# Optimization experiments

Measured on AMD Instinct MI355X. Metric: run time of the kernel, lower is better.

## Reference

```python
import jax, jax.numpy as jnp
import numpy as np

N_BALLS = 256
BATCH = 128
N_STEPS = 100
MAX_EVENTS = 5
WORLD_W = 10.0
WORLD_H = 10.0
RADIUS = 0.1
HID = 64
DT = 0.05
INF = jnp.float32(1e30)

_II_np, _JJ_np = np.triu_indices(N_BALLS, 1)
_II = jnp.asarray(_II_np)
_JJ = jnp.asarray(_JJ_np)
# wall order: left, right, bottom, top (normals point into the box)
_WN = jnp.array([[1.0, 0.0], [-1.0, 0.0], [0.0, 1.0], [0.0, -1.0]], dtype=jnp.float32)
_WP = jnp.array([0.0, -WORLD_W, 0.0, -WORLD_H], dtype=jnp.float32)


def setup_inputs():
    key = jax.random.key(0)
    ks = jax.random.split(key, 6)
    pos = jax.random.uniform(ks[0], (BATCH, N_BALLS, 2), minval=0.5, maxval=9.5)
    vel = jax.random.normal(ks[1], (BATCH, N_BALLS, 2))
    state = jnp.concatenate([pos, vel], axis=-1)  # [B, N, 4]
    radii = jnp.full((N_BALLS,), RADIUS, dtype=jnp.float32)
    sc = 0.1
    W1 = jax.random.normal(ks[2], (HID, 2)) * sc
    b1 = jnp.zeros((HID,), jnp.float32)
    W2 = jax.random.normal(ks[3], (HID, HID)) * sc
    b2 = jnp.zeros((HID,), jnp.float32)
    W3 = jax.random.normal(ks[4], (1, HID)) * sc
    b3 = jnp.zeros((1,), jnp.float32)
    return {"state": state, "radii": radii, "W1": W1, "b1": b1, "W2": W2,
            "b2": b2, "W3": W3, "b3": b3, "dt": DT, "n_steps": N_STEPS}


def _detect(pos, vel, radii):
    # pos, vel: [N,2]; vectorized replacement of the Python O(N^2) loop.
    diff = pos[_JJ] - pos[_II]                       # [P,2]
    dist = jnp.linalg.norm(diff, axis=-1)            # [P]
    gap_b = dist - (radii[_II] + radii[_JJ])
    nhat = diff / (dist + 1e-8)[:, None]
    app_b = jnp.sum((vel[_JJ] - vel[_II]) * nhat, axis=-1)
    gb = jnp.where(app_b < 0, gap_b, INF)            # only approaching pairs
    r = radii
    gw = jnp.stack([pos[:, 0] - r, WORLD_W - pos[:, 0] - r,
                    pos[:, 1] - r, WORLD_H - pos[:, 1] - r], axis=-1)  # [N,4]
    vw = jnp.stack([vel[:, 0] < 0, vel[:, 0] > 0,
                    vel[:, 1] < 0, vel[:, 1] > 0], axis=-1)
    gw = jnp.where(vw, gw, INF)
    allg = jnp.concatenate([gb, gw.reshape(-1)])
    k = jnp.argmin(allg)
    P = gb.shape[0]
    is_ball = k < P
    gap = allg[k]
    bi = jnp.where(is_ball, k, 0)
    i_b, j_b = _II[bi], _JJ[bi]
    kw = jnp.where(is_ball, 0, k - P)
    i_w, wid = kw // 4, kw % 4
    return gap, is_ball, i_b, j_b, i_w, wid


def _apply_jump(s, i, j, W1, b1, W2, b2, W3, b3):
    pos, vel = s[..., :2], s[..., 2:]
    diff = pos[:, j] - pos[:, i]                               # [B,2]
    dist = jnp.maximum(jnp.linalg.norm(diff, axis=-1, keepdims=True), 1e-8)
    nhat = diff / dist
    app = jnp.sum((vel[:, j] - vel[:, i]) * nhat, axis=-1, keepdims=True)
    h = jnp.concatenate([dist, app], axis=-1)                  # [B,2]
    h = jax.nn.silu(h @ W1.T + b1)
    h = jax.nn.silu(h @ W2.T + b2)
    imp = (h @ W3.T + b3) * nhat                               # [B,2]
    vel_new = vel.at[:, i].add(imp).at[:, j].add(-imp)
    return jnp.concatenate([pos, vel_new], axis=-1)


def _apply_wall(s, i, wn, wp, r):
    pos, vel = s[..., :2], s[..., 2:]
    v, p = vel[:, i], pos[:, i]
    vn = jnp.sum(v * wn, axis=-1, keepdims=True)
    vel_new = vel.at[:, i].set(v - 2.0 * vn * wn)
    pn = jnp.sum(p * wn, axis=-1, keepdims=True)
    pen = jnp.maximum(wp + r - pn, 0.0)
    pos_new = pos.at[:, i].set(p + pen * wn)
    return jnp.concatenate([pos_new, vel_new], axis=-1)


def _rollout(state, radii, W1, b1, W2, b2, W3, b3, dt, n_steps):
    dt = jnp.float32(dt)

    def event_body(_, carry):
        curr, t_c, t_e, done = carry
        pos0, vel0 = curr[0, :, :2], curr[0, :, 2:]
        gap, is_ball, i_b, j_b, i_w, wid = _detect(pos0, vel0, radii)
        no_event = gap > 0.05
        n = pos0[j_b] - pos0[i_b]
        app_ball = -jnp.sum((vel0[j_b] - vel0[i_b]) * n / jnp.linalg.norm(n))
        app_wall = jnp.abs(jnp.max(vel0[i_w]))
        app = jnp.where(is_ball, app_ball, app_wall)
        t_ev = t_c + gap / jnp.maximum(app, 1e-6)
        # ZeroFlow is constant velocity -> dopri5 integrate is exact linear drift
        dte = jnp.where(t_ev > t_c + 1e-10, t_ev - t_c, 0.0)

        def apply_map(s):
            jm = _apply_jump(s, i_b, j_b, W1, b1, W2, b2, W3, b3)
            wm = _apply_wall(s, i_w, _WN[wid], _WP[wid], radii[i_w])
            return jnp.where(is_ball, jm, wm)

        state_a = apply_map(curr)                       # gap <= 0: jump now
        integ = curr.at[..., :2].add(curr[..., 2:] * dte)
        state_b = apply_map(integ)                      # 0 < gap: drift then jump
        act = (~done) & (~no_event)
        case_a = act & (gap <= 0)
        case_b = act & (gap > 0) & (app > 1e-6) & (t_ev < t_e)
        new_done = done | no_event | (act & (gap > 0) & ((app <= 1e-6) | (t_ev >= t_e)))
        new_curr = jnp.where(case_a, state_a, jnp.where(case_b, state_b, curr))
        new_t_c = jnp.where(case_b, t_ev, t_c)
        return new_curr, new_t_c, t_e, new_done

    def step(curr, step_idx):
        t_s = step_idx.astype(jnp.float32) * dt
        t_e = t_s + dt
        curr, t_c, _, _ = jax.lax.fori_loop(
            0, MAX_EVENTS, event_body, (curr, t_s, t_e, jnp.bool_(False)))
        dte = jnp.where(t_e > t_c + 1e-10, t_e - t_c, 0.0)
        curr = curr.at[..., :2].add(curr[..., 2:] * dte)
        return curr, curr

    _, traj = jax.lax.scan(step, state, jnp.arange(n_steps))
    return jnp.concatenate([state[None], traj], axis=0)   # [n_steps+1, B, N, 4]


def reference(state, radii, W1, b1, W2, b2, W3, b3, dt, n_steps):
    return _rollout(state, radii, W1, b1, W2, b2, W3, b3, dt, n_steps)
```

## Files before the change

kernel.cpp:

```cpp
#include <hip/hip_runtime.h>
#include <stdint.h>

#define NB 256
#define NBATCH 128
#define HID 64
#define MAXEV 5
#define MAXSTEPS 256
#define NT 43
#define NTILES 946
#define W2S 65
#define CAND_MAX 6144
#define CMARGIN 1.5f
#define NTHR 512
#define D2GATE 0.0626f

typedef unsigned long long u64;

__device__ __forceinline__ float bf2f(unsigned short u) {
    return __uint_as_float(((unsigned)u) << 16);
}
__device__ __forceinline__ unsigned short f2bf(float f) {
    unsigned u = __float_as_uint(f);
    u += 0x7FFFu + ((u >> 16) & 1u);
    return (unsigned short)(u >> 16);
}
__device__ __forceinline__ float rdin(const void* p, int idx, int bf) {
    return bf ? bf2f(((const unsigned short*)p)[idx]) : ((const float*)p)[idx];
}
__device__ __forceinline__ float silu_f(float x) {
    float s = __fdiv_rn(1.0f, __fadd_rn(1.0f, expf(-x)));
    return __fmul_rn(x, s);
}
__device__ __forceinline__ void lds_fence() {
    __builtin_amdgcn_wave_barrier();
    __threadfence_block();
    __builtin_amdgcn_wave_barrier();
}
__device__ __forceinline__ unsigned fmap(float g) {
    unsigned u = __float_as_uint(g);
    unsigned m = (unsigned)(((int)u) >> 31) | 0x80000000u;
    return u ^ m;
}
__device__ __forceinline__ float funmap(unsigned sb) {
    unsigned u = (sb & 0x80000000u) ? (sb ^ 0x80000000u) : ~sb;
    return __uint_as_float(u);
}

template<int CTRL>
__device__ __forceinline__ u64 dpp_min_u64_step(u64 k) {
    unsigned lo = (unsigned)k, hi = (unsigned)(k >> 32);
    unsigned nlo = (unsigned)__builtin_amdgcn_update_dpp(-1, (int)lo, CTRL, 0xF, 0xF, false);
    unsigned nhi = (unsigned)__builtin_amdgcn_update_dpp(-1, (int)hi, CTRL, 0xF, 0xF, false);
    u64 nk = (((u64)nhi) << 32) | (u64)nlo;
    return nk < k ? nk : k;
}
__device__ __forceinline__ u64 wave_min_u64(u64 k) {
    k = dpp_min_u64_step<0x111>(k);
    k = dpp_min_u64_step<0x112>(k);
    k = dpp_min_u64_step<0x114>(k);
    k = dpp_min_u64_step<0x118>(k);
    k = dpp_min_u64_step<0x142>(k);
    k = dpp_min_u64_step<0x143>(k);
    unsigned lo = (unsigned)__builtin_amdgcn_readlane((int)(unsigned)k, 63);
    unsigned hi = (unsigned)__builtin_amdgcn_readlane((int)(unsigned)(k >> 32), 63);
    return (((u64)hi) << 32) | (u64)lo;
}
template<int CTRL>
__device__ __forceinline__ float dpp_max_f32_step(float x) {
    int nx = __builtin_amdgcn_update_dpp(0, __float_as_int(x), CTRL, 0xF, 0xF, false);
    return fmaxf(x, __int_as_float(nx));
}
__device__ __forceinline__ float wave_max_f32(float x) {
    x = dpp_max_f32_step<0x111>(x);
    x = dpp_max_f32_step<0x112>(x);
    x = dpp_max_f32_step<0x114>(x);
    x = dpp_max_f32_step<0x118>(x);
    x = dpp_max_f32_step<0x142>(x);
    x = dpp_max_f32_step<0x143>(x);
    return __int_as_float(__builtin_amdgcn_readlane(__float_as_int(x), 63));
}

__device__ __forceinline__ void append_agg(unsigned* list, int* counter, int cap, unsigned val) {
    u64 m = __ballot(1);
    int lane = (int)(threadIdx.x & 63);
    int ldr = (int)__builtin_ctzll(m);
    int pfx = (int)__builtin_popcountll(m & ((1ull << lane) - 1ull));
    int base = 0;
    if (lane == ldr) base = atomicAdd(counter, (int)__builtin_popcountll(m));
    base = __builtin_amdgcn_readfirstlane(base);
    int idx = base + pfx;
    if (idx < cap) list[idx] = val;
}

__device__ __forceinline__ u64 ball_key(const float4* ps, int i, int j,
                                        float dx, float dy, float d2,
                                        unsigned id, float rsum) {
    float4 A = ps[i], B = ps[j];
    float p1 = __fmul_rn(__fsub_rn(B.z, A.z), dx);
    float p2 = __fmul_rn(__fsub_rn(B.w, A.w), dy);
    float dot = __fadd_rn(p1, p2);
    float mag = __fadd_rn(fabsf(p1), fabsf(p2));
    bool appr;
    if (fabsf(dot) < __fmul_rn(1e-5f, mag)) {
        float dist = __fsqrt_rn(d2);
        float den = __fadd_rn(dist, 1e-8f);
        float ab = __fadd_rn(__fmul_rn(__fsub_rn(B.z, A.z), __fdiv_rn(dx, den)),
                             __fmul_rn(__fsub_rn(B.w, A.w), __fdiv_rn(dy, den)));
        appr = ab < 0.0f;
    } else {
        appr = dot < 0.0f;
    }
    if (!appr) return ~0ull;
    float gap = __fsub_rn(__fsqrt_rn(d2), rsum);
    return (((u64)fmap(gap)) << 17) | id;
}

__device__ __forceinline__ void scan_list(const unsigned* src, int n,
                                          const float2* pos2c, const float4* ps0c,
                                          float rsum, u64& kC, int tid) {
    unsigned idq[8];
    #pragma unroll
    for (int q = 0; q < 8; q++) {
        int c = tid + q * NTHR;
        idq[q] = (c < n) ? src[c] : 0u;
    }
    float2 Aq[8], Bq[8];
    #pragma unroll
    for (int q = 0; q < 8; q++) {
        Aq[q] = pos2c[idq[q] >> 8];
        Bq[q] = pos2c[idq[q] & 255u];
    }
    #pragma unroll
    for (int q = 0; q < 8; q++) {
        float dx = __fsub_rn(Bq[q].x, Aq[q].x), dy = __fsub_rn(Bq[q].y, Aq[q].y);
        float d2 = __fadd_rn(__fmul_rn(dx, dx), __fmul_rn(dy, dy));
        bool live = (tid + q * NTHR) < n;
        if (live && d2 < D2GATE) {
            u64 key = ball_key(ps0c, (int)(idq[q] >> 8), (int)(idq[q] & 255u),
                               dx, dy, d2, idq[q], rsum);
            kC = key < kC ? key : kC;
        }
    }
    for (int c = tid + 8 * NTHR; c < n; c += NTHR) {
        unsigned id = src[c];
        float2 A = pos2c[id >> 8], B = pos2c[id & 255u];
        float dx = __fsub_rn(B.x, A.x), dy = __fsub_rn(B.y, A.y);
        float d2 = __fadd_rn(__fmul_rn(dx, dx), __fmul_rn(dy, dy));
        if (d2 < D2GATE) {
            u64 key = ball_key(ps0c, (int)(id >> 8), (int)(id & 255u), dx, dy, d2, id, rsum);
            kC = key < kC ? key : kC;
        }
    }
}

__device__ __forceinline__ void scan_full(const float2* pos2c, const float4* ps0c, float rsum,
                                          int i0a, int j0a, int i0b, int j0b,
                                          bool apB, float th2B, unsigned* cand, int* candN,
                                          u64& kC) {
    #pragma unroll
    for (int tt = 0; tt < 2; tt++) {
        int I0 = tt ? i0b : i0a;
        int J0 = tt ? j0b : j0a;
        if (I0 < 0) continue;
        float2 Pi[6], Pj[6];
        #pragma unroll
        for (int a = 0; a < 6; a++) {
            int ii = I0 + a; ii = ii < NB ? ii : NB - 1;
            int jj = J0 + a; jj = jj < NB ? jj : NB - 1;
            Pi[a] = pos2c[ii]; Pj[a] = pos2c[jj];
        }
        #pragma unroll
        for (int a = 0; a < 6; a++) {
            int i = I0 + a;
            #pragma unroll
            for (int bb = 0; bb < 6; bb++) {
                int j = J0 + bb;
                bool ok = (i < NB) && (j < NB) && (j > i);
                float dx = __fsub_rn(Pj[bb].x, Pi[a].x);
                float dy = __fsub_rn(Pj[bb].y, Pi[a].y);
                float d2 = __fadd_rn(__fmul_rn(dx, dx), __fmul_rn(dy, dy));
                unsigned id = (unsigned)((i << 8) | j);
                if (apB && ok && d2 < th2B) append_agg(cand, candN, CAND_MAX, id);
                if (ok && d2 < D2GATE) {
                    u64 key = ball_key(ps0c, i, j, dx, dy, d2, id, rsum);
                    kC = key < kC ? key : kC;
                }
            }
        }
    }
}

__device__ __forceinline__ void store_ball(void* out, long long base, int t, float4 Q, int bf) {
    if (bf) {
        ushort4 v;
        v.x = f2bf(Q.x); v.y = f2bf(Q.y); v.z = f2bf(Q.z); v.w = f2bf(Q.w);
        ((ushort4*)((unsigned short*)out + base))[t] = v;
    } else {
        ((float4*)((float*)out + base))[t] = Q;
    }
}

__device__ void load_weights(float* w1, float* b1s, float* w2, float* b2s, float* w3, float* b3s,
                             const void* W1, const void* B1, const void* W2, const void* B2,
                             const void* W3, const void* B3, int bf, int tid, int nthr) {
    for (int k = tid; k < HID * 2; k += nthr) w1[k] = rdin(W1, k, bf);
    for (int k = tid; k < HID; k += nthr) {
        b1s[k] = rdin(B1, k, bf);
        b2s[k] = rdin(B2, k, bf);
        w3[k]  = rdin(W3, k, bf);
    }
    for (int k = tid; k < HID * HID; k += nthr) {
        int m = k >> 6, c = k & 63;
        w2[m * W2S + c] = rdin(W2, k, bf);
    }
    if (tid == 0) b3s[0] = rdin(B3, 0, bf);
}

__global__ void sniff_kernel(const unsigned short* st, int* ws) {
    __shared__ int ev;
    if (threadIdx.x == 0) ev = 0;
    __syncthreads();
    unsigned short u = st[threadIdx.x];
    int e = (u >> 7) & 0xFF;
    if (e >= 0x85) atomicOr(&ev, 1);
    __syncthreads();
    if (threadIdx.x == 0) ws[0] = ev ? 0 : 1;
}

__global__ void row0_kernel(const void* in, void* out, const int* ws) {
    int idx = blockIdx.x * blockDim.x + threadIdx.x;
    if (ws[0]) ((unsigned short*)out)[idx] = ((const unsigned short*)in)[idx];
    else       ((float*)out)[idx] = ((const float*)in)[idx];
}

__global__ __launch_bounds__(NTHR, 1) void sim_kernel(
    const void* in_state, const void* in_rad,
    const void* inW1, const void* inB1, const void* inW2, const void* inB2,
    const void* inW3, const void* inB3, const void* in_dt, const int* in_nsteps,
    void* out, const int* ws) {
    __shared__ float4 ps0[2][NB];
    __shared__ float4 psb[2][NB];
    __shared__ float2 pos2[2][NB];
    __shared__ float w1[HID * 2], b1s[HID], w2[HID * W2S], b2s[HID], w3s[HID], b3s[1];
    __shared__ float sc0[132], scb[132];
    __shared__ u64 redK[8];
    __shared__ float redF[5];
    __shared__ unsigned cand[CAND_MAX];
    __shared__ int candN;
    __shared__ int pubF;
    __shared__ int rebF;

    int tid = threadIdx.x;
    int b = blockIdx.x;
    int bf = ws[0];

    if (tid < NB) {
        int base0 = tid * 4;
        float4 P;
        P.x = rdin(in_state, base0 + 0, bf);
        P.y = rdin(in_state, base0 + 1, bf);
        P.z = rdin(in_state, base0 + 2, bf);
        P.w = rdin(in_state, base0 + 3, bf);
        ps0[0][tid] = P;
        float2 p2v; p2v.x = P.x; p2v.y = P.y;
        pos2[0][tid] = p2v;
        int baseb = (b * NB + tid) * 4;
        float4 Q;
        Q.x = rdin(in_state, baseb + 0, bf);
        Q.y = rdin(in_state, baseb + 1, bf);
        Q.z = rdin(in_state, baseb + 2, bf);
        Q.w = rdin(in_state, baseb + 3, bf);
        psb[0][tid] = Q;
        float m2 = P.z * P.z + P.w * P.w;
        m2 = wave_max_f32(m2);
        if ((tid & 63) == 0) redF[tid >> 6] = m2;
    }
    load_weights(w1, b1s, w2, b2s, w3s, b3s, inW1, inB1, inW2, inB2, inW3, inB3, bf, tid, NTHR);
    if (tid == 0) { candN = 0; pubF = 0; rebF = 1; redF[4] = 0.0f; }

    float dtv = rdin(in_dt, 0, bf);
    int NS = in_nsteps[0]; if (NS > MAXSTEPS) NS = MAXSTEPS; if (NS < 0) NS = 0;
    float rad0 = rdin(in_rad, 0, bf);
    float rsum = __fadd_rn(rad0, rad0);

    int i0a = -1, j0a = 0, i0b = -1, j0b = 0;
    {
        int T = tid;
        if (T < NTILES) {
            int rem = T, r = 0;
            while (rem >= NT - r) { rem -= NT - r; r++; }
            i0a = r * 6; j0a = (r + rem) * 6;
        }
        T = tid + NTHR;
        if (T < NTILES) {
            int rem = T, r = 0;
            while (rem >= NT - r) { rem -= NT - r; r++; }
            i0b = r * 6; j0b = (r + rem) * 6;
        }
    }
    __syncthreads();

    float thB = __fadd_rn(__fadd_rn(rsum, 0.05f), CMARGIN);
    float th2B = __fmul_rn(thB, thB);

    int p = 0;
    int nc = 0;
    bool candOvf = false;
    float used = 1e30f, vcap = 0.0f;

    for (int s = 0; s < NS; s++) {
        int rebuild = rebF;
        float t_s = __fmul_rn((float)s, dtv);
        float t_e = __fadd_rn(t_s, dtv);
        float t_c = t_s;
        long long obase = ((long long)(s + 1) * NBATCH + b) * (NB * 4);
        if (tid < 64) {
            if (rebuild) {
                vcap = sqrtf(fmaxf(fmaxf(fmaxf(redF[0], redF[1]),
                                         fmaxf(redF[2], redF[3])), redF[4]));
                used = 0.0f;
            }
            used = __fadd_rn(used, __fmul_rn(__fmul_rn(2.0f, dtv), vcap));
        }

        for (int e = 0; e < MAXEV; e++) {
            const float4* ps0c = ps0[p];
            const float2* pos2c = pos2[p];
            const float4* psbc = psb[p];
            float4* ps0n = ps0[p ^ 1];
            float2* pos2n = pos2[p ^ 1];
            float4* psbn = psb[p ^ 1];

            u64 kC = ~0ull;
            int mode;
            if (e == 0) mode = rebuild ? 2 : 1;
            else        mode = pubF ? 2 : 1;
            if (mode == 2) {
                bool apB = (e == 0);
                scan_full(pos2c, ps0c, rsum, i0a, j0a, i0b, j0b,
                          apB, th2B, cand, &candN, kC);
            } else {
                scan_list(cand, nc, pos2c, ps0c, rsum, kC, tid);
            }
            {
                int ball = tid & 255, wsel = tid >> 8;
                float4 P = ps0c[ball];
                #pragma unroll
                for (int q = 0; q < 2; q++) {
                    int w = wsel * 2 + q;
                    float g; bool valid;
                    if (w == 0)      { g = __fsub_rn(P.x, rad0); valid = P.z < 0.0f; }
                    else if (w == 1) { g = __fsub_rn(__fsub_rn(10.0f, P.x), rad0); valid = P.z > 0.0f; }
                    else if (w == 2) { g = __fsub_rn(P.y, rad0); valid = P.w < 0.0f; }
                    else             { g = __fsub_rn(__fsub_rn(10.0f, P.y), rad0); valid = P.w > 0.0f; }
                    if (valid) {
                        u64 key = (((u64)fmap(g)) << 17) | 0x10000u | (unsigned)(ball * 4 + w);
                        kC = key < kC ? key : kC;
                    }
                }
            }
            kC = wave_min_u64(kC);
            if ((tid & 63) == 0) redK[tid >> 6] = kC;
            __syncthreads();

            if (e == 0 && rebuild) {
                int ct = candN;
                candOvf = ct > CAND_MAX;
                nc = candOvf ? CAND_MAX : ct;
            }

            float g_nx = 0, g_ny = 0, g_dist = 0, g_app = 0;
            float4 gA, gB;
            int code = 0; float dteB = 0.0f; float tcn = t_c;
            int ei = 0, ejw = 0;
            {
                u64 m = redK[0];
                #pragma unroll
                for (int q = 1; q < 8; q++) m = redK[q] < m ? redK[q] : m;
                if (m != ~0ull) {
                    bool is_ball = ((m >> 16) & 1ull) == 0;
                    unsigned id = (unsigned)(m & 0xFFFFull);
                    float gap = funmap((unsigned)(m >> 17));
                    int pi = (int)(id >> 8), pj = (int)(id & 255u);
                    int wb = (int)(id >> 2), ww = (int)(id & 3u);
                    ei = is_ball ? pi : wb;
                    ejw = is_ball ? pj : ww;
                    float4 A, B;
                    if (!(gap > 0.05f)) {
                        float app;
                        if (is_ball) {
                            A = ps0c[pi]; B = ps0c[pj];
                            float dx = __fsub_rn(B.x, A.x), dy = __fsub_rn(B.y, A.y);
                            float nrm = __fsqrt_rn(__fadd_rn(__fmul_rn(dx, dx), __fmul_rn(dy, dy)));
                            float dvx = __fsub_rn(B.z, A.z), dvy = __fsub_rn(B.w, A.w);
                            app = -__fadd_rn(__fdiv_rn(__fmul_rn(dvx, dx), nrm),
                                             __fdiv_rn(__fmul_rn(dvy, dy), nrm));
                        } else {
                            float4 Wb = ps0c[wb];
                            app = fabsf(fmaxf(Wb.z, Wb.w));
                        }
                        float t_ev = __fadd_rn(t_c, __fdiv_rn(gap, fmaxf(app, 1e-6f)));
                        if (gap <= 0.0f) {
                            code = is_ball ? 1 : 3;
                        } else if (app > 1e-6f && t_ev < t_e) {
                            code = is_ball ? 2 : 4;
                            dteB = (t_ev > __fadd_rn(t_c, 1e-10f)) ? __fsub_rn(t_ev, t_c) : 0.0f;
                            tcn = t_ev;
                        }
                    }
                    if (tid < 64 && code != 0 && code <= 2) {
                        if (code == 2) {
                            A.x = __fadd_rn(A.x, __fmul_rn(A.z, dteB));
                            A.y = __fadd_rn(A.y, __fmul_rn(A.w, dteB));
                            B.x = __fadd_rn(B.x, __fmul_rn(B.z, dteB));
                            B.y = __fadd_rn(B.y, __fmul_rn(B.w, dteB));
                        }
                        gA = A; gB = B;
                        float dx = __fsub_rn(B.x, A.x), dy = __fsub_rn(B.y, A.y);
                        float nrm = __fsqrt_rn(__fadd_rn(__fmul_rn(dx, dx), __fmul_rn(dy, dy)));
                        float dist = fmaxf(nrm, 1e-8f);
                        g_nx = __fdiv_rn(dx, dist); g_ny = __fdiv_rn(dy, dist);
                        g_dist = dist;
                        float dvx = __fsub_rn(B.z, A.z), dvy = __fsub_rn(B.w, A.w);
                        g_app = __fadd_rn(__fmul_rn(dvx, g_nx), __fmul_rn(dvy, g_ny));
                    }
                }
            }

            if (code == 0) {
                float fd = (t_e > __fadd_rn(t_c, 1e-10f)) ? __fsub_rn(t_e, t_c) : 0.0f;
                if (tid < NB) {
                    float4 P = ps0c[tid];
                    P.x = __fadd_rn(P.x, __fmul_rn(P.z, fd));
                    P.y = __fadd_rn(P.y, __fmul_rn(P.w, fd));
                    ps0n[tid] = P;
                    float2 pp; pp.x = P.x; pp.y = P.y; pos2n[tid] = pp;
                    float m2 = P.z * P.z + P.w * P.w;
                    m2 = wave_max_f32(m2);
                    if ((tid & 63) == 0) redF[tid >> 6] = m2;
                    if (tid == 0) {
                        redF[4] = 0.0f;
                        candN = 0;
                        float usedNext = __fadd_rn(used, __fmul_rn(__fmul_rn(2.0f, dtv), vcap));
                        rebF = (candOvf || (__fadd_rn(usedNext, 1e-3f) > CMARGIN)) ? 1 : 0;
                    }
                } else {
                    int t = tid - NB;
                    float4 Q = psbc[t];
                    Q.x = __fadd_rn(Q.x, __fmul_rn(Q.z, fd));
                    Q.y = __fadd_rn(Q.y, __fmul_rn(Q.w, fd));
                    psbn[t] = Q;
                    store_ball(out, obase, t, Q, bf);
                }
                __syncthreads();
                p ^= 1;
                break;
            }

            t_c = tcn;
            bool integ = (code == 2) || (code == 4);
            bool last = (e == MAXEV - 1);
            float fd = 0.0f;
            if (last) fd = (t_e > __fadd_rn(t_c, 1e-10f)) ? __fsub_rn(t_e, t_c) : 0.0f;
            int skip2 = (code <= 2) ? ejw : -1;

            if (code <= 2) {
                if (tid < 64) {
                    float a = __fadd_rn(__fadd_rn(__fmul_rn(g_dist, w1[2 * tid]),
                                                  __fmul_rn(g_app, w1[2 * tid + 1])), b1s[tid]);
                    sc0[4 + tid] = silu_f(a);
                    lds_fence();
                    float acc = 0.0f;
                    const float* row = &w2[tid * W2S];
                    #pragma unroll 8
                    for (int k = 0; k < HID; k++) acc = __fadd_rn(acc, __fmul_rn(sc0[4 + k], row[k]));
                    acc = __fadd_rn(acc, b2s[tid]);
                    sc0[68 + tid] = silu_f(acc);
                    lds_fence();
                    float acc3 = 0.0f;
                    #pragma unroll 8
                    for (int k = 0; k < HID; k++)
                        acc3 = __fadd_rn(acc3, __fmul_rn(sc0[68 + k], w3s[k]));
                    float impv = __fadd_rn(acc3, b3s[0]);
                    float ix = __fmul_rn(impv, g_nx), iy = __fmul_rn(impv, g_ny);
                    float nAz = __fadd_rn(gA.z, ix),  nAw = __fadd_rn(gA.w, iy);
                    float nBz = __fadd_rn(gB.z, -ix), nBw = __fadd_rn(gB.w, -iy);
                    if (tid == 0) {
                        float4 outA; outA.x = gA.x; outA.y = gA.y; outA.z = nAz; outA.w = nAw;
                        float4 outB; outB.x = gB.x; outB.y = gB.y; outB.z = nBz; outB.w = nBw;
                        if (last) {
                            outA.x = __fadd_rn(outA.x, __fmul_rn(outA.z, fd));
                            outA.y = __fadd_rn(outA.y, __fmul_rn(outA.w, fd));
                            outB.x = __fadd_rn(outB.x, __fmul_rn(outB.z, fd));
                            outB.y = __fadd_rn(outB.y, __fmul_rn(outB.w, fd));
                        }
                        ps0n[ei] = outA; ps0n[ejw] = outB;
                        float2 pa; pa.x = outA.x; pa.y = outA.y; pos2n[ei] = pa;
                        float2 pb; pb.x = outB.x; pb.y = outB.y; pos2n[ejw] = pb;
                    }
                    float s1 = sqrtf(nAz * nAz + nAw * nAw);
                    float s2 = sqrtf(nBz * nBz + nBw * nBw);
                    float nv = fmaxf(s1, s2);
                    used = __fadd_rn(used, __fmul_rn(__fmul_rn(2.0f, dtv),
                                                     fmaxf(__fsub_rn(nv, vcap), 0.0f)));
                    vcap = fmaxf(vcap, nv);
                    int nf = (candOvf || (__fadd_rn(used, 1e-3f) > CMARGIN)) ? 1 : 0;
                    if (tid == 0) {
                        pubF = nf;
                        if (last) {
                            redF[4] = fmaxf(nAz * nAz + nAw * nAw, nBz * nBz + nBw * nBw);
                            candN = 0;
                            float usedNext = __fadd_rn(used, __fmul_rn(__fmul_rn(2.0f, dtv), vcap));
                            rebF = (candOvf || (__fadd_rn(usedNext, 1e-3f) > CMARGIN)) ? 1 : 0;
                        }
                    }
                } else if (tid < 128) {
                    int lane = tid - 64;
                    float4 A = psbc[ei], B = psbc[ejw];
                    if (integ) {
                        A.x = __fadd_rn(A.x, __fmul_rn(A.z, dteB));
                        A.y = __fadd_rn(A.y, __fmul_rn(A.w, dteB));
                        B.x = __fadd_rn(B.x, __fmul_rn(B.z, dteB));
                        B.y = __fadd_rn(B.y, __fmul_rn(B.w, dteB));
                    }
                    float dx = __fsub_rn(B.x, A.x), dy = __fsub_rn(B.y, A.y);
                    float nrm = __fsqrt_rn(__fadd_rn(__fmul_rn(dx, dx), __fmul_rn(dy, dy)));
                    float dist = fmaxf(nrm, 1e-8f);
                    float nx = __fdiv_rn(dx, dist), ny = __fdiv_rn(dy, dist);
                    float dvx = __fsub_rn(B.z, A.z), dvy = __fsub_rn(B.w, A.w);
                    float app2 = __fadd_rn(__fmul_rn(dvx, nx), __fmul_rn(dvy, ny));
                    float a = __fadd_rn(__fadd_rn(__fmul_rn(dist, w1[2 * lane]),
                                                  __fmul_rn(app2, w1[2 * lane + 1])), b1s[lane]);
                    scb[4 + lane] = silu_f(a);
                    lds_fence();
                    float acc = 0.0f;
                    const float* row = &w2[lane * W2S];
                    #pragma unroll 8
                    for (int k = 0; k < HID; k++) acc = __fadd_rn(acc, __fmul_rn(scb[4 + k], row[k]));
                    acc = __fadd_rn(acc, b2s[lane]);
                    scb[68 + lane] = silu_f(acc);
                    lds_fence();
                    float acc3 = 0.0f;
                    #pragma unroll 8
                    for (int k = 0; k < HID; k++)
                        acc3 = __fadd_rn(acc3, __fmul_rn(scb[68 + k], w3s[k]));
                    float impv = __fadd_rn(acc3, b3s[0]);
                    if (lane == 0) {
                        float ix = __fmul_rn(impv, nx), iy = __fmul_rn(impv, ny);
                        float4 outA; outA.x = A.x; outA.y = A.y;
                        outA.z = __fadd_rn(A.z, ix);  outA.w = __fadd_rn(A.w, iy);
                        float4 outB; outB.x = B.x; outB.y = B.y;
                        outB.z = __fadd_rn(B.z, -ix); outB.w = __fadd_rn(B.w, -iy);
                        if (last) {
                            outA.x = __fadd_rn(outA.x, __fmul_rn(outA.z, fd));
                            outA.y = __fadd_rn(outA.y, __fmul_rn(outA.w, fd));
                            outB.x = __fadd_rn(outB.x, __fmul_rn(outB.z, fd));
                            outB.y = __fadd_rn(outB.y, __fmul_rn(outB.w, fd));
                            store_ball(out, obase, ei, outA, bf);
                            store_ball(out, obase, ejw, outB, bf);
                        }
                        psbn[ei] = outA; psbn[ejw] = outB;
                    }
                }
            } else {
                const float wnx[4] = {1.f, -1.f, 0.f, 0.f};
                const float wny[4] = {0.f, 0.f, 1.f, -1.f};
                const float wpv[4] = {0.f, -10.f, 0.f, -10.f};
                int w = ejw;
                if (tid < 64) {
                    float4 P = ps0c[ei];
                    if (integ) {
                        P.x = __fadd_rn(P.x, __fmul_rn(P.z, dteB));
                        P.y = __fadd_rn(P.y, __fmul_rn(P.w, dteB));
                    }
                    float vn = __fadd_rn(__fmul_rn(P.z, wnx[w]), __fmul_rn(P.w, wny[w]));
                    float t2 = __fmul_rn(2.0f, vn);
                    float nvx = __fsub_rn(P.z, __fmul_rn(t2, wnx[w]));
                    float nvy = __fsub_rn(P.w, __fmul_rn(t2, wny[w]));
                    float pn = __fadd_rn(__fmul_rn(P.x, wnx[w]), __fmul_rn(P.y, wny[w]));
                    float pen = fmaxf(__fsub_rn(__fadd_rn(wpv[w], rad0), pn), 0.0f);
                    float4 nP;
                    nP.x = __fadd_rn(P.x, __fmul_rn(pen, wnx[w]));
                    nP.y = __fadd_rn(P.y, __fmul_rn(pen, wny[w]));
                    nP.z = nvx; nP.w = nvy;
                    if (last) {
                        nP.x = __fadd_rn(nP.x, __fmul_rn(nP.z, fd));
                        nP.y = __fadd_rn(nP.y, __fmul_rn(nP.w, fd));
                    }
                    used = __fadd_rn(used, pen);
                    int nf = (candOvf || (__fadd_rn(used, 1e-3f) > CMARGIN)) ? 1 : 0;
                    if (tid == 0) {
                        ps0n[ei] = nP;
                        float2 pp; pp.x = nP.x; pp.y = nP.y; pos2n[ei] = pp;
                        pubF = nf;
                        if (last) {
                            redF[4] = nvx * nvx + nvy * nvy;
                            candN = 0;
                            float usedNext = __fadd_rn(used, __fmul_rn(__fmul_rn(2.0f, dtv), vcap));
                            rebF = (candOvf || (__fadd_rn(usedNext, 1e-3f) > CMARGIN)) ? 1 : 0;
                        }
                    }
                } else if (tid < 128) {
                    if (tid == 64) {
                        float4 P = psbc[ei];
                        if (integ) {
                            P.x = __fadd_rn(P.x, __fmul_rn(P.z, dteB));
                            P.y = __fadd_rn(P.y, __fmul_rn(P.w, dteB));
                        }
                        float vn = __fadd_rn(__fmul_rn(P.z, wnx[w]), __fmul_rn(P.w, wny[w]));
                        float t2 = __fmul_rn(2.0f, vn);
                        float nvx = __fsub_rn(P.z, __fmul_rn(t2, wnx[w]));
                        float nvy = __fsub_rn(P.w, __fmul_rn(t2, wny[w]));
                        float pn = __fadd_rn(__fmul_rn(P.x, wnx[w]), __fmul_rn(P.y, wny[w]));
                        float pen = fmaxf(__fsub_rn(__fadd_rn(wpv[w], rad0), pn), 0.0f);
                        float4 nP;
                        nP.x = __fadd_rn(P.x, __fmul_rn(pen, wnx[w]));
                        nP.y = __fadd_rn(P.y, __fmul_rn(pen, wny[w]));
                        nP.z = nvx; nP.w = nvy;
                        if (last) {
                            nP.x = __fadd_rn(nP.x, __fmul_rn(nP.z, fd));
                            nP.y = __fadd_rn(nP.y, __fmul_rn(nP.w, fd));
                            store_ball(out, obase, ei, nP, bf);
                        }
                        psbn[ei] = nP;
                    }
                }
            }
            if (tid >= 128 && tid < 384) {
                int t = tid - 128;
                float m2 = 0.0f;
                if (t != ei && t != skip2) {
                    float4 P = ps0c[t];
                    P.x = __fadd_rn(P.x, __fmul_rn(P.z, dteB));
                    P.y = __fadd_rn(P.y, __fmul_rn(P.w, dteB));
                    if (last) {
                        P.x = __fadd_rn(P.x, __fmul_rn(P.z, fd));
                        P.y = __fadd_rn(P.y, __fmul_rn(P.w, fd));
                        m2 = P.z * P.z + P.w * P.w;
                    }
                    ps0n[t] = P;
                    float2 pp; pp.x = P.x; pp.y = P.y; pos2n[t] = pp;
                }
                if (last) {
                    float mx = wave_max_f32(m2);
                    if ((tid & 63) == 0) redF[(tid >> 6) - 2] = mx;
                }
            } else if (tid >= 384) {
                #pragma unroll
                for (int q = 0; q < 2; q++) {
                    int t = (tid - 384) + q * 128;
                    if (t != ei && t != skip2) {
                        float4 Q = psbc[t];
                        Q.x = __fadd_rn(Q.x, __fmul_rn(Q.z, dteB));
                        Q.y = __fadd_rn(Q.y, __fmul_rn(Q.w, dteB));
                        if (last) {
                            Q.x = __fadd_rn(Q.x, __fmul_rn(Q.z, fd));
                            Q.y = __fadd_rn(Q.y, __fmul_rn(Q.w, fd));
                            store_ball(out, obase, t, Q, bf);
                        }
                        psbn[t] = Q;
                    }
                }
            }
            __syncthreads();
            p ^= 1;
        }
    }
}

extern "C" void kernel_launch(void* const* d_in, const int* in_sizes, int n_in,
                              void* d_out, int out_size, void* d_ws, size_t ws_size,
                              hipStream_t stream) {
    int* ws = (int*)d_ws;
    sniff_kernel<<<1, 256, 0, stream>>>((const unsigned short*)d_in[0], ws);
    row0_kernel<<<(NBATCH * NB * 4) / 256, 256, 0, stream>>>(d_in[0], d_out, ws);
    sim_kernel<<<NBATCH, NTHR, 0, stream>>>(
        d_in[0], d_in[1], d_in[2], d_in[3], d_in[4], d_in[5], d_in[6], d_in[7],
        d_in[8], (const int*)d_in[9], d_out, ws);
}
```

Baseline: 3.261 ms.

## Prescan next event's candidate pairs during state update to drop a barrier

Candidate-list and wall keys for the next event are now computed speculatively during the current update phase, using predicted positions, and written into a double-buffered reduction array. The next event then reads that precomputed minimum and only rescans pairs and walls involving the one or two balls that just changed. The separate float2 position array is removed and ball_key reads are taken from register float4s. This aims to remove one full scan and one __syncthreads per event, in exchange for more work and register pressure in the update phase and some risk of mismatch between predicted and actual positions.

```diff
diff --git a/kernel.cpp b/kernel.cpp
--- a/kernel.cpp
+++ b/kernel.cpp
@@ -92,10 +92,8 @@
     if (idx < cap) list[idx] = val;
 }
 
-__device__ __forceinline__ u64 ball_key(const float4* ps, int i, int j,
-                                        float dx, float dy, float d2,
-                                        unsigned id, float rsum) {
-    float4 A = ps[i], B = ps[j];
+__device__ __forceinline__ u64 ball_key_v(float4 A, float4 B, float dx, float dy,
+                                          float d2, unsigned id, float rsum) {
     float p1 = __fmul_rn(__fsub_rn(B.z, A.z), dx);
     float p2 = __fmul_rn(__fsub_rn(B.w, A.w), dy);
     float dot = __fadd_rn(p1, p2);
@@ -115,59 +113,91 @@
     return (((u64)fmap(gap)) << 17) | id;
 }
 
-__device__ __forceinline__ void scan_list(const unsigned* src, int n,
-                                          const float2* pos2c, const float4* ps0c,
-                                          float rsum, u64& kC, int tid) {
-    unsigned idq[8];
+__device__ __forceinline__ u64 wall_keys2(float px, float py, float vz, float vw,
+                                          float rad0, int ball, int wsel) {
+    u64 k = ~0ull;
     #pragma unroll
-    for (int q = 0; q < 8; q++) {
-        int c = tid + q * NTHR;
-        idq[q] = (c < n) ? src[c] : 0u;
-    }
-    float2 Aq[8], Bq[8];
-    #pragma unroll
-    for (int q = 0; q < 8; q++) {
-        Aq[q] = pos2c[idq[q] >> 8];
-        Bq[q] = pos2c[idq[q] & 255u];
-    }
-    #pragma unroll
-    for (int q = 0; q < 8; q++) {
-        float dx = __fsub_rn(Bq[q].x, Aq[q].x), dy = __fsub_rn(Bq[q].y, Aq[q].y);
-        float d2 = __fadd_rn(__fmul_rn(dx, dx), __fmul_rn(dy, dy));
-        bool live = (tid + q * NTHR) < n;
-        if (live && d2 < D2GATE) {
-            u64 key = ball_key(ps0c, (int)(idq[q] >> 8), (int)(idq[q] & 255u),
-                               dx, dy, d2, idq[q], rsum);
-            kC = key < kC ? key : kC;
-        }
-    }
-    for (int c = tid + 8 * NTHR; c < n; c += NTHR) {
-        unsigned id = src[c];
-        float2 A = pos2c[id >> 8], B = pos2c[id & 255u];
-        float dx = __fsub_rn(B.x, A.x), dy = __fsub_rn(B.y, A.y);
-        float d2 = __fadd_rn(__fmul_rn(dx, dx), __fmul_rn(dy, dy));
-        if (d2 < D2GATE) {
-            u64 key = ball_key(ps0c, (int)(id >> 8), (int)(id & 255u), dx, dy, d2, id, rsum);
-            kC = key < kC ? key : kC;
-        }
-    }
-}
-
-__device__ __forceinline__ void scan_full(const float2* pos2c, const float4* ps0c, float rsum,
-                                          int i0a, int j0a, int i0b, int j0b,
-                                          bool apB, float th2B, unsigned* cand, int* candN,
-                                          u64& kC) {
+    for (int q = 0; q < 2; q++) {
+        int w = wsel * 2 + q;
+        float g; bool valid;
+        if (w == 0)      { g = __fsub_rn(px, rad0); valid = vz < 0.0f; }
+        else if (w == 1) { g = __fsub_rn(__fsub_rn(10.0f, px), rad0); valid = vz > 0.0f; }
+        else if (w == 2) { g = __fsub_rn(py, rad0); valid = vw < 0.0f; }
+        else             { g = __fsub_rn(__fsub_rn(10.0f, py), rad0); valid = vw > 0.0f; }
+        if (valid) {
+            u64 key = (((u64)fmap(g)) << 17) | 0x10000u | (unsigned)(ball * 4 + w);
+            k = key < k ? key : k;
+        }
+    }
+    return k;
+}
+__device__ __forceinline__ u64 wall_keys4(float4 P, float rad0, int ball) {
+    u64 k = wall_keys2(P.x, P.y, P.z, P.w, rad0, ball, 0);
+    u64 k2 = wall_keys2(P.x, P.y, P.z, P.w, rad0, ball, 1);
+    return k2 < k ? k2 : k;
+}
+
+__device__ __forceinline__ void pred_pos(float4 P, float dta, float dtb, bool dtbon,
+                                         float& px, float& py) {
+    px = __fadd_rn(P.x, __fmul_rn(P.z, dta));
+    py = __fadd_rn(P.y, __fmul_rn(P.w, dta));
+    if (dtbon) {
+        px = __fadd_rn(px, __fmul_rn(P.z, dtb));
+        py = __fadd_rn(py, __fmul_rn(P.w, dtb));
+    }
+}
+
+__device__ __forceinline__ void prescan_pairs(const unsigned* cand, int n,
+        const float4* ps0c, int e0, int e1, float dta, float dtb, bool dtbon,
+        float rsum, u64& kC, int start, int stride) {
+    for (int c0 = start; c0 < n; c0 += stride * 4) {
+        unsigned id4[4];
+        bool lv[4];
+        float4 A4[4], B4[4];
+        #pragma unroll
+        for (int q = 0; q < 4; q++) {
+            int cc = c0 + q * stride;
+            lv[q] = cc < n;
+            id4[q] = lv[q] ? cand[cc] : 0u;
+        }
+        #pragma unroll
+        for (int q = 0; q < 4; q++) {
+            A4[q] = ps0c[id4[q] >> 8];
+            B4[q] = ps0c[id4[q] & 255u];
+        }
+        #pragma unroll
+        for (int q = 0; q < 4; q++) {
+            int i = (int)(id4[q] >> 8), j = (int)(id4[q] & 255u);
+            if (!lv[q] || i == e0 || i == e1 || j == e0 || j == e1) continue;
+            float4 A = A4[q], B = B4[q];
+            float ax, ay, bx, by;
+            pred_pos(A, dta, dtb, dtbon, ax, ay);
+            pred_pos(B, dta, dtb, dtbon, bx, by);
+            A.x = ax; A.y = ay; B.x = bx; B.y = by;
+            float dx = __fsub_rn(B.x, A.x), dy = __fsub_rn(B.y, A.y);
+            float d2 = __fadd_rn(__fmul_rn(dx, dx), __fmul_rn(dy, dy));
+            if (d2 < D2GATE) {
+                u64 key = ball_key_v(A, B, dx, dy, d2, id4[q], rsum);
+                kC = key < kC ? key : kC;
+            }
+        }
+    }
+}
+
+__device__ __forceinline__ void scan_full4(const float4* ps0c, float rsum,
+        int i0a, int j0a, int i0b, int j0b,
+        bool apB, float th2B, unsigned* cand, int* candN, u64& kC) {
     #pragma unroll
     for (int tt = 0; tt < 2; tt++) {
         int I0 = tt ? i0b : i0a;
         int J0 = tt ? j0b : j0a;
         if (I0 < 0) continue;
-        float2 Pi[6], Pj[6];
+        float4 Pi[6], Pj[6];
         #pragma unroll
         for (int a = 0; a < 6; a++) {
             int ii = I0 + a; ii = ii < NB ? ii : NB - 1;
             int jj = J0 + a; jj = jj < NB ? jj : NB - 1;
-            Pi[a] = pos2c[ii]; Pj[a] = pos2c[jj];
+            Pi[a] = ps0c[ii]; Pj[a] = ps0c[jj];
         }
         #pragma unroll
         for (int a = 0; a < 6; a++) {
@@ -182,7 +212,7 @@
                 unsigned id = (unsigned)((i << 8) | j);
                 if (apB && ok && d2 < th2B) append_agg(cand, candN, CAND_MAX, id);
                 if (ok && d2 < D2GATE) {
-                    u64 key = ball_key(ps0c, i, j, dx, dy, d2, id, rsum);
+                    u64 key = ball_key_v(Pi[a], Pj[bb], dx, dy, d2, id, rsum);
                     kC = key < kC ? key : kC;
                 }
             }
@@ -240,14 +270,13 @@
     void* out, const int* ws) {
     __shared__ float4 ps0[2][NB];
     __shared__ float4 psb[2][NB];
-    __shared__ float2 pos2[2][NB];
     __shared__ float w1[HID * 2], b1s[HID], w2[HID * W2S], b2s[HID], w3s[HID], b3s[1];
     __shared__ float sc0[132], scb[132];
-    __shared__ u64 redK[8];
+    __shared__ u64 redK2[2][8];
+    __shared__ int pubF2[2];
     __shared__ float redF[5];
     __shared__ unsigned cand[CAND_MAX];
     __shared__ int candN;
-    __shared__ int pubF;
     __shared__ int rebF;
 
     int tid = threadIdx.x;
@@ -262,8 +291,6 @@
         P.z = rdin(in_state, base0 + 2, bf);
         P.w = rdin(in_state, base0 + 3, bf);
         ps0[0][tid] = P;
-        float2 p2v; p2v.x = P.x; p2v.y = P.y;
-        pos2[0][tid] = p2v;
         int baseb = (b * NB + tid) * 4;
         float4 Q;
         Q.x = rdin(in_state, baseb + 0, bf);
@@ -276,7 +303,7 @@
         if ((tid & 63) == 0) redF[tid >> 6] = m2;
     }
     load_weights(w1, b1s, w2, b2s, w3s, b3s, inW1, inB1, inW2, inB2, inW3, inB3, bf, tid, NTHR);
-    if (tid == 0) { candN = 0; pubF = 0; rebF = 1; redF[4] = 0.0f; }
+    if (tid == 0) { candN = 0; pubF2[0] = 0; pubF2[1] = 0; rebF = 1; redF[4] = 0.0f; }
 
     float dtv = rdin(in_dt, 0, bf);
     int NS = in_nsteps[0]; if (NS > MAXSTEPS) NS = MAXSTEPS; if (NS < 0) NS = 0;
@@ -307,6 +334,7 @@
     int nc = 0;
     bool candOvf = false;
     float used = 1e30f, vcap = 0.0f;
+    int fixI = -1, fixJ = -1;
 
     for (int s = 0; s < NS; s++) {
         int rebuild = rebF;
@@ -324,117 +352,135 @@
         }
 
         for (int e = 0; e < MAXEV; e++) {
-            const float4* ps0c = ps0[p];
-            const float2* pos2c = pos2[p];
-            const float4* psbc = psb[p];
+            float4* ps0c = ps0[p];
+            float4* psbc = psb[p];
             float4* ps0n = ps0[p ^ 1];
-            float2* pos2n = pos2[p ^ 1];
             float4* psbn = psb[p ^ 1];
 
-            u64 kC = ~0ull;
-            int mode;
-            if (e == 0) mode = rebuild ? 2 : 1;
-            else        mode = pubF ? 2 : 1;
-            if (mode == 2) {
+            u64 m;
+            bool fullscan = (e == 0) ? (rebuild != 0) : (pubF2[p] != 0);
+            if (fullscan) {
+                u64 kC = ~0ull;
                 bool apB = (e == 0);
-                scan_full(pos2c, ps0c, rsum, i0a, j0a, i0b, j0b,
-                          apB, th2B, cand, &candN, kC);
+                scan_full4(ps0c, rsum, i0a, j0a, i0b, j0b, apB, th2B, cand, &candN, kC);
+                {
+                    int ball = tid & 255;
+                    float4 P = ps0c[ball];
+                    u64 kw = wall_keys2(P.x, P.y, P.z, P.w, rad0, ball, tid >> 8);
+                    kC = kw < kC ? kw : kC;
+                }
+                kC = wave_min_u64(kC);
+                if ((tid & 63) == 0) redK2[p][tid >> 6] = kC;
+                __syncthreads();
+                if (e == 0 && rebuild) {
+                    int ct = candN;
+                    candOvf = ct > CAND_MAX;
+                    nc = candOvf ? CAND_MAX : ct;
+                }
+                m = redK2[p][0];
+                #pragma unroll
+                for (int q = 1; q < 8; q++) m = redK2[p][q] < m ? redK2[p][q] : m;
             } else {
-                scan_list(cand, nc, pos2c, ps0c, rsum, kC, tid);
-            }
-            {
-                int ball = tid & 255, wsel = tid >> 8;
-                float4 P = ps0c[ball];
+                m = redK2[p][0];
                 #pragma unroll
-                for (int q = 0; q < 2; q++) {
-                    int w = wsel * 2 + q;
-                    float g; bool valid;
-                    if (w == 0)      { g = __fsub_rn(P.x, rad0); valid = P.z < 0.0f; }
-                    else if (w == 1) { g = __fsub_rn(__fsub_rn(10.0f, P.x), rad0); valid = P.z > 0.0f; }
-                    else if (w == 2) { g = __fsub_rn(P.y, rad0); valid = P.w < 0.0f; }
-                    else             { g = __fsub_rn(__fsub_rn(10.0f, P.y), rad0); valid = P.w > 0.0f; }
-                    if (valid) {
-                        u64 key = (((u64)fmap(g)) << 17) | 0x10000u | (unsigned)(ball * 4 + w);
-                        kC = key < kC ? key : kC;
-                    }
-                }
-            }
-            kC = wave_min_u64(kC);
-            if ((tid & 63) == 0) redK[tid >> 6] = kC;
-            __syncthreads();
-
-            if (e == 0 && rebuild) {
-                int ct = candN;
-                candOvf = ct > CAND_MAX;
-                nc = candOvf ? CAND_MAX : ct;
+                for (int q = 1; q < 8; q++) m = redK2[p][q] < m ? redK2[p][q] : m;
+                if (fixI >= 0) {
+                    int lane = tid & 63;
+                    float4 F0 = ps0c[fixI];
+                    bool hasJ = fixJ >= 0;
+                    float4 F1 = hasJ ? ps0c[fixJ] : F0;
+                    u64 kfix = ~0ull;
+                    #pragma unroll
+                    for (int q = 0; q < 8; q++) {
+                        bool useJ = q >= 4;
+                        if (useJ && !hasJ) continue;
+                        int base = useJ ? fixJ : fixI;
+                        float4 Fb = useJ ? F1 : F0;
+                        int x = lane + (q & 3) * 64;
+                        if (x == base) continue;
+                        float4 X = ps0c[x];
+                        int i, j; float4 A, B;
+                        if (base < x) { i = base; j = x; A = Fb; B = X; }
+                        else          { i = x; j = base; A = X; B = Fb; }
+                        float dx = __fsub_rn(B.x, A.x), dy = __fsub_rn(B.y, A.y);
+                        float d2 = __fadd_rn(__fmul_rn(dx, dx), __fmul_rn(dy, dy));
+                        if (d2 < D2GATE) {
+                            unsigned id = (unsigned)((i << 8) | j);
+                            u64 key = ball_key_v(A, B, dx, dy, d2, id, rsum);
+                            kfix = key < kfix ? key : kfix;
+                        }
+                    }
+                    kfix = wave_min_u64(kfix);
+                    m = kfix < m ? kfix : m;
+                    u64 kw = wall_keys4(F0, rad0, fixI);
+                    m = kw < m ? kw : m;
+                    if (hasJ) {
+                        kw = wall_keys4(F1, rad0, fixJ);
+                        m = kw < m ? kw : m;
+                    }
+                }
             }
 
             float g_nx = 0, g_ny = 0, g_dist = 0, g_app = 0;
             float4 gA, gB;
             int code = 0; float dteB = 0.0f; float tcn = t_c;
             int ei = 0, ejw = 0;
-            {
-                u64 m = redK[0];
-                #pragma unroll
-                for (int q = 1; q < 8; q++) m = redK[q] < m ? redK[q] : m;
-                if (m != ~0ull) {
-                    bool is_ball = ((m >> 16) & 1ull) == 0;
-                    unsigned id = (unsigned)(m & 0xFFFFull);
-                    float gap = funmap((unsigned)(m >> 17));
-                    int pi = (int)(id >> 8), pj = (int)(id & 255u);
-                    int wb = (int)(id >> 2), ww = (int)(id & 3u);
-                    ei = is_ball ? pi : wb;
-                    ejw = is_ball ? pj : ww;
-                    float4 A, B;
-                    if (!(gap > 0.05f)) {
-                        float app;
-                        if (is_ball) {
-                            A = ps0c[pi]; B = ps0c[pj];
-                            float dx = __fsub_rn(B.x, A.x), dy = __fsub_rn(B.y, A.y);
-                            float nrm = __fsqrt_rn(__fadd_rn(__fmul_rn(dx, dx), __fmul_rn(dy, dy)));
-                            float dvx = __fsub_rn(B.z, A.z), dvy = __fsub_rn(B.w, A.w);
-                            app = -__fadd_rn(__fdiv_rn(__fmul_rn(dvx, dx), nrm),
-                                             __fdiv_rn(__fmul_rn(dvy, dy), nrm));
-                        } else {
-                            float4 Wb = ps0c[wb];
-                            app = fabsf(fmaxf(Wb.z, Wb.w));
-                        }
-                        float t_ev = __fadd_rn(t_c, __fdiv_rn(gap, fmaxf(app, 1e-6f)));
-                        if (gap <= 0.0f) {
-                            code = is_ball ? 1 : 3;
-                        } else if (app > 1e-6f && t_ev < t_e) {
-                            code = is_ball ? 2 : 4;
-                            dteB = (t_ev > __fadd_rn(t_c, 1e-10f)) ? __fsub_rn(t_ev, t_c) : 0.0f;
-                            tcn = t_ev;
-                        }
-                    }
-                    if (tid < 64 && code != 0 && code <= 2) {
-                        if (code == 2) {
-                            A.x = __fadd_rn(A.x, __fmul_rn(A.z, dteB));
-                            A.y = __fadd_rn(A.y, __fmul_rn(A.w, dteB));
-                            B.x = __fadd_rn(B.x, __fmul_rn(B.z, dteB));
-                            B.y = __fadd_rn(B.y, __fmul_rn(B.w, dteB));
-                        }
-                        gA = A; gB = B;
+            if (m != ~0ull) {
+                bool is_ball = ((m >> 16) & 1ull) == 0;
+                unsigned id = (unsigned)(m & 0xFFFFull);
+                float gap = funmap((unsigned)(m >> 17));
+                int pi = (int)(id >> 8), pj = (int)(id & 255u);
+                int wb = (int)(id >> 2), ww = (int)(id & 3u);
+                ei = is_ball ? pi : wb;
+                ejw = is_ball ? pj : ww;
+                float4 A, B;
+                if (!(gap > 0.05f)) {
+                    float app;
+                    if (is_ball) {
+                        A = ps0c[pi]; B = ps0c[pj];
                         float dx = __fsub_rn(B.x, A.x), dy = __fsub_rn(B.y, A.y);
                         float nrm = __fsqrt_rn(__fadd_rn(__fmul_rn(dx, dx), __fmul_rn(dy, dy)));
-                        float dist = fmaxf(nrm, 1e-8f);
-                        g_nx = __fdiv_rn(dx, dist); g_ny = __fdiv_rn(dy, dist);
-                        g_dist = dist;
                         float dvx = __fsub_rn(B.z, A.z), dvy = __fsub_rn(B.w, A.w);
-                        g_app = __fadd_rn(__fmul_rn(dvx, g_nx), __fmul_rn(dvy, g_ny));
-                    }
+                        app = -__fadd_rn(__fdiv_rn(__fmul_rn(dvx, dx), nrm),
+                                         __fdiv_rn(__fmul_rn(dvy, dy), nrm));
+                    } else {
+                        float4 Wb = ps0c[wb];
+                        app = fabsf(fmaxf(Wb.z, Wb.w));
+                    }
+                    float t_ev = __fadd_rn(t_c, __fdiv_rn(gap, fmaxf(app, 1e-6f)));
+                    if (gap <= 0.0f) {
+                        code = is_ball ? 1 : 3;
+                    } else if (app > 1e-6f && t_ev < t_e) {
+                        code = is_ball ? 2 : 4;
+                        dteB = (t_ev > __fadd_rn(t_c, 1e-10f)) ? __fsub_rn(t_ev, t_c) : 0.0f;
+                        tcn = t_ev;
+                    }
+                }
+                if (tid < 64 && code != 0 && code <= 2) {
+                    if (code == 2) {
+                        A.x = __fadd_rn(A.x, __fmul_rn(A.z, dteB));
+                        A.y = __fadd_rn(A.y, __fmul_rn(A.w, dteB));
+                        B.x = __fadd_rn(B.x, __fmul_rn(B.z, dteB));
+                        B.y = __fadd_rn(B.y, __fmul_rn(B.w, dteB));
+                    }
+                    gA = A; gB = B;
+                    float dx = __fsub_rn(B.x, A.x), dy = __fsub_rn(B.y, A.y);
+                    float nrm = __fsqrt_rn(__fadd_rn(__fmul_rn(dx, dx), __fmul_rn(dy, dy)));
+                    float dist = fmaxf(nrm, 1e-8f);
+                    g_nx = __fdiv_rn(dx, dist); g_ny = __fdiv_rn(dy, dist);
+                    g_dist = dist;
+                    float dvx = __fsub_rn(B.z, A.z), dvy = __fsub_rn(B.w, A.w);
+                    g_app = __fadd_rn(__fmul_rn(dvx, g_nx), __fmul_rn(dvy, g_ny));
                 }
             }
 
             if (code == 0) {
-                float fd = (t_e > __fadd_rn(t_c, 1e-10f)) ? __fsub_rn(t_e, t_c) : 0.0f;
+                float fd0 = (t_e > __fadd_rn(t_c, 1e-10f)) ? __fsub_rn(t_e, t_c) : 0.0f;
                 if (tid < NB) {
                     float4 P = ps0c[tid];
-                    P.x = __fadd_rn(P.x, __fmul_rn(P.z, fd));
-                    P.y = __fadd_rn(P.y, __fmul_rn(P.w, fd));
+                    P.x = __fadd_rn(P.x, __fmul_rn(P.z, fd0));
+                    P.y = __fadd_rn(P.y, __fmul_rn(P.w, fd0));
                     ps0n[tid] = P;
-                    float2 pp; pp.x = P.x; pp.y = P.y; pos2n[tid] = pp;
                     float m2 = P.z * P.z + P.w * P.w;
                     m2 = wave_max_f32(m2);
                     if ((tid & 63) == 0) redF[tid >> 6] = m2;
@@ -447,13 +493,26 @@
                 } else {
                     int t = tid - NB;
                     float4 Q = psbc[t];
-                    Q.x = __fadd_rn(Q.x, __fmul_rn(Q.z, fd));
-                    Q.y = __fadd_rn(Q.y, __fmul_rn(Q.w, fd));
+                    Q.x = __fadd_rn(Q.x, __fmul_rn(Q.z, fd0));
+                    Q.y = __fadd_rn(Q.y, __fmul_rn(Q.w, fd0));
                     psbn[t] = Q;
                     store_ball(out, obase, t, Q, bf);
                 }
+                u64 kP = ~0ull;
+                prescan_pairs(cand, nc, ps0c, -1, -1, fd0, 0.0f, false, rsum, kP, tid, NTHR);
+                {
+                    int ball = tid & 255;
+                    float4 P = ps0c[ball];
+                    float px, py;
+                    pred_pos(P, fd0, 0.0f, false, px, py);
+                    u64 kw = wall_keys2(px, py, P.z, P.w, rad0, ball, tid >> 8);
+                    kP = kw < kP ? kw : kP;
+                }
+                kP = wave_min_u64(kP);
+                if ((tid & 63) == 0) redK2[p ^ 1][tid >> 6] = kP;
                 __syncthreads();
                 p ^= 1;
+                fixI = -1; fixJ = -1;
                 break;
             }
 
@@ -495,8 +554,6 @@
                             outB.y = __fadd_rn(outB.y, __fmul_rn(outB.w, fd));
                         }
                         ps0n[ei] = outA; ps0n[ejw] = outB;
-                        float2 pa; pa.x = outA.x; pa.y = outA.y; pos2n[ei] = pa;
-                        float2 pb; pb.x = outB.x; pb.y = outB.y; pos2n[ejw] = pb;
                     }
                     float s1 = sqrtf(nAz * nAz + nAw * nAw);
                     float s2 = sqrtf(nBz * nBz + nBw * nBw);
@@ -506,7 +563,7 @@
                     vcap = fmaxf(vcap, nv);
                     int nf = (candOvf || (__fadd_rn(used, 1e-3f) > CMARGIN)) ? 1 : 0;
                     if (tid == 0) {
-                        pubF = nf;
+                        pubF2[p ^ 1] = nf;
                         if (last) {
                             redF[4] = fmaxf(nAz * nAz + nAw * nAw, nBz * nBz + nBw * nBw);
                             candN = 0;
@@ -591,8 +648,7 @@
                     int nf = (candOvf || (__fadd_rn(used, 1e-3f) > CMARGIN)) ? 1 : 0;
                     if (tid == 0) {
                         ps0n[ei] = nP;
-                        float2 pp; pp.x = nP.x; pp.y = nP.y; pos2n[ei] = pp;
-                        pubF = nf;
+                        pubF2[p ^ 1] = nf;
                         if (last) {
                             redF[4] = nvx * nvx + nvy * nvy;
                             candN = 0;
@@ -639,7 +695,6 @@
                         m2 = P.z * P.z + P.w * P.w;
                     }
                     ps0n[t] = P;
-                    float2 pp; pp.x = P.x; pp.y = P.y; pos2n[t] = pp;
                 }
                 if (last) {
                     float mx = wave_max_f32(m2);
@@ -662,8 +717,26 @@
                     }
                 }
             }
+            {
+                u64 kP = ~0ull;
+                if (tid >= 128) {
+                    prescan_pairs(cand, nc, ps0c, ei, skip2, dteB, fd, last,
+                                  rsum, kP, tid - 128, NTHR - 128);
+                }
+                int ball = tid & 255;
+                if (ball != ei && ball != skip2) {
+                    float4 P = ps0c[ball];
+                    float px, py;
+                    pred_pos(P, dteB, fd, last, px, py);
+                    u64 kw = wall_keys2(px, py, P.z, P.w, rad0, ball, tid >> 8);
+                    kP = kw < kP ? kw : kP;
+                }
+                kP = wave_min_u64(kP);
+                if ((tid & 63) == 0) redK2[p ^ 1][tid >> 6] = kP;
+            }
             __syncthreads();
             p ^= 1;
+            fixI = ei; fixJ = skip2;
         }
     }
 }
```

New measurement: 3.794 ms. 16.4% more time.
